# Kernel tuning notes

Measured on AMD Instinct MI355X. Metric: run time of the kernel, lower is better.

The kernel has to match this reference:

```python
import jax, jax.numpy as jnp
import numpy as np

BLOCK = (16, 16)  # (block rows over out_features, block cols over in_features)
TOKENS, IN_F, OUT_F = 8192, 4096, 4096


def setup_inputs() -> dict:
    key = jax.random.key(0)
    k1, k2, k3, k4 = jax.random.split(key, 4)
    x = jax.random.normal(k1, (TOKENS, IN_F), dtype=jnp.float32)
    weight = jax.random.normal(k2, (OUT_F, IN_F), dtype=jnp.float32) / np.sqrt(IN_F)
    bias = jax.random.normal(k3, (OUT_F,), dtype=jnp.float32)
    block_mask = jax.random.bernoulli(k4, 0.5, (OUT_F // BLOCK[0], IN_F // BLOCK[1]))
    return {"x": x, "weight": weight, "bias": bias, "block_mask": block_mask}


def _expand_mask(block_mask, dtype):
    # [X, Y] block mask -> [out_features, in_features] dense 0/1 mask
    m = jnp.repeat(block_mask, BLOCK[0], axis=0)
    m = jnp.repeat(m, BLOCK[1], axis=1)
    return m.astype(dtype)


def reference(x, weight, bias, block_mask):
    # Sparse path: block-sparse matmul with the block-masked weight
    # (blocksparseMM(sparse_data, x, block_size) == x @ (W * mask).T)
    w_sparse = weight * _expand_mask(block_mask, weight.dtype)
    x_sparse = jnp.einsum('ti,oi->to', x, w_sparse)
    # Dense residual path: standard linear with the full weight + bias
    x_dense = jnp.einsum('ti,oi->to', x, weight) + bias
    return x_sparse + x_dense
```

## Files before the change

### kernel.cpp

```cpp
#include <hip/hip_runtime.h>
#include <hip/hip_bf16.h>
#include <stdint.h>

#define TOKENS 8192
#define IN_F   4096
#define OUT_F  4096

typedef __attribute__((ext_vector_type(4))) float  f32x4;
typedef __attribute__((ext_vector_type(8))) __bf16 bf16x8;

__device__ __forceinline__ unsigned short f2bf(float f) {
    union { float f; uint32_t u; } c; c.f = f;
    uint32_t u = c.u;
    u += 0x7fffu + ((u >> 16) & 1);
    return (unsigned short)(u >> 16);
}

__device__ __forceinline__ void load_lds_16(const void* gptr, void* lptr) {
    __builtin_amdgcn_global_load_lds(
        (const __attribute__((address_space(1))) unsigned int*)gptr,
        (__attribute__((address_space(3))) unsigned int*)lptr, 16, 0, 0);
}

template<int N> __device__ __forceinline__ void vm_bar() {
    if constexpr (N == 6)      asm volatile("s_waitcnt vmcnt(6)\ns_barrier" ::: "memory");
    else if constexpr (N == 5) asm volatile("s_waitcnt vmcnt(5)\ns_barrier" ::: "memory");
    else if constexpr (N == 4) asm volatile("s_waitcnt vmcnt(4)\ns_barrier" ::: "memory");
    else if constexpr (N == 3) asm volatile("s_waitcnt vmcnt(3)\ns_barrier" ::: "memory");
    else if constexpr (N == 2) asm volatile("s_waitcnt vmcnt(2)\ns_barrier" ::: "memory");
    else if constexpr (N == 1) asm volatile("s_waitcnt vmcnt(1)\ns_barrier" ::: "memory");
    else                       asm volatile("s_waitcnt vmcnt(0)\ns_barrier" ::: "memory");
}

__global__ __launch_bounds__(256) void cvt_x_kernel(const float* __restrict__ x,
                                                    unsigned short* __restrict__ xb, int n4) {
    int i = blockIdx.x * blockDim.x + threadIdx.x;
    int stride = gridDim.x * blockDim.x;
    for (; i < n4; i += stride) {
        float4 v = ((const float4*)x)[i];
        ushort4 o;
        o.x = f2bf(v.x); o.y = f2bf(v.y); o.z = f2bf(v.z); o.w = f2bf(v.w);
        ((ushort4*)xb)[i] = o;
    }
}

__global__ __launch_bounds__(256) void cvt_w_kernel(const float* __restrict__ w,
                                                    const int* __restrict__ mask,
                                                    unsigned short* __restrict__ wb) {
    const int n4 = OUT_F * IN_F / 4;
    int i = blockIdx.x * blockDim.x + threadIdx.x;
    int stride = gridDim.x * blockDim.x;
    for (; i < n4; i += stride) {
        int elem = i * 4;
        int o = elem >> 12;
        int k = elem & (IN_F - 1);
        int mb = mask[(o >> 4) * (IN_F / 16) + (k >> 4)];
        float s = mb ? 2.0f : 1.0f;
        float4 v = ((const float4*)w)[i];
        ushort4 ov;
        ov.x = f2bf(v.x * s); ov.y = f2bf(v.y * s);
        ov.z = f2bf(v.z * s); ov.w = f2bf(v.w * s);
        ((ushort4*)wb)[i] = ov;
    }
}

#define BM 256
#define BN 256
#define BK 64
#define TILE_SH (BM * BK)

#define PHASE_MFMA(P)                                                          \
    {                                                                          \
        bf16x8 b0 = *(const bf16x8*)(pB + boff0 + (P) * 1024);                 \
        bf16x8 b1 = *(const bf16x8*)(pB + boff1 + (P) * 1024);                 \
        __builtin_amdgcn_s_setprio(1);                                         \
        _Pragma("unroll")                                                      \
        for (int mf = 0; mf < 8; ++mf) {                                       \
            acc[mf][P] = __builtin_amdgcn_mfma_f32_16x16x32_bf16(a[mf][0], b0, acc[mf][P], 0, 0, 0); \
            acc[mf][P] = __builtin_amdgcn_mfma_f32_16x16x32_bf16(a[mf][1], b1, acc[mf][P], 0, 0, 0); \
        }                                                                      \
        __builtin_amdgcn_s_setprio(0);                                         \
    }

#define KTILE(STG, V0, V1, V2, V3)                                             \
    {                                                                          \
        vm_bar<V0>();                                                          \
        if (STG) {                                                             \
            load_lds_16(cgA, stA + dA);                                        \
            load_lds_16(cgA + (size_t)64 * IN_F, stA + dA + 4096);             \
        }                                                                      \
        _Pragma("unroll")                                                      \
        for (int mf = 0; mf < 8; ++mf) {                                       \
            a[mf][0] = *(const bf16x8*)(pA + aoff0 + mf * 1024);               \
            a[mf][1] = *(const bf16x8*)(pA + aoff1 + mf * 1024);               \
        }                                                                      \
        PHASE_MFMA(0)                                                          \
        vm_bar<V1>();                                                          \
        if (STG) {                                                             \
            load_lds_16(cgA + (size_t)128 * IN_F, stA + dA + 8192);            \
            load_lds_16(cgA + (size_t)192 * IN_F, stA + dA + 12288);           \
        }                                                                      \
        PHASE_MFMA(1)                                                          \
        vm_bar<V2>();                                                          \
        if (STG) {                                                             \
            load_lds_16(cgB, stB + dB);                                        \
            load_lds_16(cgB + (size_t)16 * IN_F, stB + dB + 1024);             \
        }                                                                      \
        PHASE_MFMA(2)                                                          \
        vm_bar<V3>();                                                          \
        if (STG) {                                                             \
            load_lds_16(cgB + (size_t)32 * IN_F, stB + dB + 2048);             \
            load_lds_16(cgB + (size_t)48 * IN_F, stB + dB + 3072);             \
        }                                                                      \
        PHASE_MFMA(3)                                                          \
    }

__global__ __launch_bounds__(512, 2) void gemm8_kernel(const unsigned short* __restrict__ A,
                                                       const unsigned short* __restrict__ B,
                                                       const float* __restrict__ bias,
                                                       float* __restrict__ C) {
    extern __shared__ __align__(16) unsigned short sm[];

    const int tid  = threadIdx.x;
    const int lane = tid & 63;
    const int wid  = tid >> 6;
    const int wr   = wid >> 2;
    const int wc   = wid & 3;

    const int nwg = (TOKENS / BM) * (OUT_F / BN);
    int bid = blockIdx.x;
    int swz = (bid & 7) * (nwg >> 3) + (bid >> 3);
    const int tiles_n = OUT_F / BN;
    const int t0 = (swz / tiles_n) * BM;
    const int o0 = (swz % tiles_n) * BN;

    const int srow = tid >> 3;
    const int lc   = (tid & 7) ^ (srow & 7);
    const unsigned short* gA = A + (size_t)(t0 + srow) * IN_F + lc * 8;
    const int growb = (wid >> 1) * 64 + (wid & 1) * 8 + (lane >> 3);
    const unsigned short* gB = B + (size_t)(o0 + growb) * IN_F + lc * 8;
    const int dA = tid * 8;
    const int dB = growb * 64 + (tid & 7) * 8;

    const int l15 = lane & 15, q = lane >> 4, l7 = lane & 7;
    const int aoff0 = (wr * 128 + l15) * 64 + (q ^ l7) * 8;
    const int aoff1 = (wr * 128 + l15) * 64 + ((4 + q) ^ l7) * 8;
    const int boff0 = (wc * 64 + l15) * 64 + (q ^ l7) * 8;
    const int boff1 = (wc * 64 + l15) * 64 + ((4 + q) ^ l7) * 8;

    f32x4 acc[8][4];
#pragma unroll
    for (int i = 0; i < 8; ++i)
#pragma unroll
        for (int j = 0; j < 4; ++j) acc[i][j] = (f32x4)0.0f;

#pragma unroll
    for (int r = 0; r < 4; ++r)
        load_lds_16(gA + (size_t)r * 64 * IN_F, sm + dA + r * 4096);
#pragma unroll
    for (int j = 0; j < 4; ++j)
        load_lds_16(gB + (size_t)j * 16 * IN_F, sm + 2 * TILE_SH + dB + j * 1024);

    bf16x8 a[8][2];

    const unsigned short* cgA = gA + BK;
    const unsigned short* cgB = gB + BK;
    for (int kt = 0; kt < IN_F / BK - 1; ++kt) {
        const int cur = kt & 1, nxt = (kt + 1) & 1;
        const unsigned short* pA = sm + cur * TILE_SH;
        const unsigned short* pB = sm + 2 * TILE_SH + cur * TILE_SH;
        unsigned short* stA = sm + nxt * TILE_SH;
        unsigned short* stB = sm + 2 * TILE_SH + nxt * TILE_SH;
        KTILE(true, 3, 4, 5, 6)
        cgA += BK; cgB += BK;
    }
    {
        const unsigned short* pA = sm + TILE_SH;
        const unsigned short* pB = sm + 2 * TILE_SH + TILE_SH;
        unsigned short* stA = sm;
        unsigned short* stB = sm + 2 * TILE_SH;
        KTILE(false, 3, 2, 1, 0)
        (void)stA; (void)stB;
    }

    float bv[4];
#pragma unroll
    for (int nf = 0; nf < 4; ++nf) bv[nf] = bias[o0 + wc * 64 + nf * 16 + l15];
#pragma unroll
    for (int mf = 0; mf < 8; ++mf) {
        const int t = t0 + wr * 128 + mf * 16 + q * 4;
#pragma unroll
        for (int nf = 0; nf < 4; ++nf) {
            const int o = o0 + wc * 64 + nf * 16 + l15;
#pragma unroll
            for (int r = 0; r < 4; ++r)
                C[(size_t)(t + r) * OUT_F + o] = acc[mf][nf][r] + bv[nf];
        }
    }
}

__global__ __launch_bounds__(256) void gemm_f32_fallback(const float* __restrict__ x,
                                                         const float* __restrict__ w,
                                                         const float* __restrict__ bias,
                                                         const int* __restrict__ mask,
                                                         float* __restrict__ out) {
    __shared__ float As[64][17];
    __shared__ float Bs[64][17];
    int bid = blockIdx.x;
    const int tiles_n = OUT_F / 64;
    int tm = bid / tiles_n, tn = bid % tiles_n;
    int t0 = tm * 64, o0 = tn * 64;
    int tid = threadIdx.x;
    int tx = tid & 15, ty = tid >> 4;
    int lrow = tid >> 2, lc4 = (tid & 3) * 4;
    float acc[4][4] = {};
    for (int k0 = 0; k0 < IN_F; k0 += 16) {
        float4 av = *(const float4*)&x[(size_t)(t0 + lrow) * IN_F + k0 + lc4];
        float4 bv = *(const float4*)&w[(size_t)(o0 + lrow) * IN_F + k0 + lc4];
        int mb = mask[((o0 + lrow) >> 4) * (IN_F / 16) + ((k0 + lc4) >> 4)];
        float s = mb ? 2.0f : 1.0f;
        As[lrow][lc4 + 0] = av.x; As[lrow][lc4 + 1] = av.y;
        As[lrow][lc4 + 2] = av.z; As[lrow][lc4 + 3] = av.w;
        Bs[lrow][lc4 + 0] = bv.x * s; Bs[lrow][lc4 + 1] = bv.y * s;
        Bs[lrow][lc4 + 2] = bv.z * s; Bs[lrow][lc4 + 3] = bv.w * s;
        __syncthreads();
#pragma unroll
        for (int kk = 0; kk < 16; ++kk) {
            float av2[4], bv2[4];
#pragma unroll
            for (int i = 0; i < 4; ++i) av2[i] = As[ty * 4 + i][kk];
#pragma unroll
            for (int j = 0; j < 4; ++j) bv2[j] = Bs[tx * 4 + j][kk];
#pragma unroll
            for (int i = 0; i < 4; ++i)
#pragma unroll
                for (int j = 0; j < 4; ++j) acc[i][j] += av2[i] * bv2[j];
        }
        __syncthreads();
    }
#pragma unroll
    for (int j = 0; j < 4; ++j) {
        int o = o0 + tx * 4 + j;
        float bv = bias[o];
#pragma unroll
        for (int i = 0; i < 4; ++i)
            out[(size_t)(t0 + ty * 4 + i) * OUT_F + o] = acc[i][j] + bv;
    }
}

extern "C" void kernel_launch(void* const* d_in, const int* in_sizes, int n_in,
                              void* d_out, int out_size, void* d_ws, size_t ws_size,
                              hipStream_t stream) {
    const float* x    = (const float*)d_in[0];
    const float* wgt  = (const float*)d_in[1];
    const float* bias = (const float*)d_in[2];
    const int*   mask = (const int*)d_in[3];
    float* out = (float*)d_out;

    size_t xb_bytes = (size_t)TOKENS * IN_F * 2;
    size_t wb_bytes = (size_t)OUT_F * IN_F * 2;

    if (ws_size >= xb_bytes + wb_bytes) {
        unsigned short* xb = (unsigned short*)d_ws;
        unsigned short* wb = (unsigned short*)((char*)d_ws + xb_bytes);
        hipLaunchKernelGGL(cvt_x_kernel, dim3(2048), dim3(256), 0, stream, x, xb, TOKENS * IN_F / 4);
        hipLaunchKernelGGL(cvt_w_kernel, dim3(1024), dim3(256), 0, stream, wgt, mask, wb);
        (void)hipFuncSetAttribute((const void*)gemm8_kernel,
                                  hipFuncAttributeMaxDynamicSharedMemorySize, 131072);
        hipLaunchKernelGGL(gemm8_kernel, dim3((TOKENS / BM) * (OUT_F / BN)), dim3(512),
                           131072, stream, xb, wb, bias, out);
    } else {
        hipLaunchKernelGGL(gemm_f32_fallback, dim3((TOKENS / 64) * (OUT_F / 64)), dim3(256), 0, stream,
                           x, wgt, bias, mask, out);
    }
}
```

Baseline: 280.0 us.

## Restructure GEMM main loop into half-K sub-tiles with finer-grained LDS pipeline

Reorganizes the LDS layout into 32-wide K halves with a new XOR swizzle. The main loop becomes a ping-pong schedule: each sub-step issues fragment reads, then the async global-to-LDS load for a future half-tile, then 16 MFMAs fenced by barriers, keeping three half-tiles in flight. The aim is to hide global latency and LDS reads behind MFMA work while cutting register pressure from the previously held 16 A fragments. It adds many more barriers per K-tile, which could cost synchronization overhead.

```diff
diff --git a/kernel.cpp b/kernel.cpp
--- a/kernel.cpp
+++ b/kernel.cpp
@@ -22,13 +22,14 @@
         (__attribute__((address_space(3))) unsigned int*)lptr, 16, 0, 0);
 }
 
-template<int N> __device__ __forceinline__ void vm_bar() {
-    if constexpr (N == 6)      asm volatile("s_waitcnt vmcnt(6)\ns_barrier" ::: "memory");
-    else if constexpr (N == 5) asm volatile("s_waitcnt vmcnt(5)\ns_barrier" ::: "memory");
-    else if constexpr (N == 4) asm volatile("s_waitcnt vmcnt(4)\ns_barrier" ::: "memory");
-    else if constexpr (N == 3) asm volatile("s_waitcnt vmcnt(3)\ns_barrier" ::: "memory");
-    else if constexpr (N == 2) asm volatile("s_waitcnt vmcnt(2)\ns_barrier" ::: "memory");
-    else if constexpr (N == 1) asm volatile("s_waitcnt vmcnt(1)\ns_barrier" ::: "memory");
+__device__ __forceinline__ void open_bar() {
+    asm volatile("s_barrier\ns_waitcnt lgkmcnt(0)" ::: "memory");
+    __builtin_amdgcn_sched_barrier(0);
+}
+__device__ __forceinline__ void cbar() { asm volatile("s_barrier" ::: "memory"); }
+template<int W> __device__ __forceinline__ void cbar_w() {
+    if constexpr (W == 8)      asm volatile("s_waitcnt vmcnt(8)\ns_barrier" ::: "memory");
+    else if constexpr (W == 4) asm volatile("s_waitcnt vmcnt(4)\ns_barrier" ::: "memory");
     else                       asm volatile("s_waitcnt vmcnt(0)\ns_barrier" ::: "memory");
 }
 
@@ -67,53 +68,64 @@
 #define BM 256
 #define BN 256
 #define BK 64
-#define TILE_SH (BM * BK)
-
-#define PHASE_MFMA(P)                                                          \
-    {                                                                          \
-        bf16x8 b0 = *(const bf16x8*)(pB + boff0 + (P) * 1024);                 \
-        bf16x8 b1 = *(const bf16x8*)(pB + boff1 + (P) * 1024);                 \
-        __builtin_amdgcn_s_setprio(1);                                         \
-        _Pragma("unroll")                                                      \
-        for (int mf = 0; mf < 8; ++mf) {                                       \
-            acc[mf][P] = __builtin_amdgcn_mfma_f32_16x16x32_bf16(a[mf][0], b0, acc[mf][P], 0, 0, 0); \
-            acc[mf][P] = __builtin_amdgcn_mfma_f32_16x16x32_bf16(a[mf][1], b1, acc[mf][P], 0, 0, 0); \
-        }                                                                      \
-        __builtin_amdgcn_s_setprio(0);                                         \
-    }
-
-#define KTILE(STG, V0, V1, V2, V3)                                             \
-    {                                                                          \
-        vm_bar<V0>();                                                          \
-        if (STG) {                                                             \
-            load_lds_16(cgA, stA + dA);                                        \
-            load_lds_16(cgA + (size_t)64 * IN_F, stA + dA + 4096);             \
-        }                                                                      \
-        _Pragma("unroll")                                                      \
-        for (int mf = 0; mf < 8; ++mf) {                                       \
-            a[mf][0] = *(const bf16x8*)(pA + aoff0 + mf * 1024);               \
-            a[mf][1] = *(const bf16x8*)(pA + aoff1 + mf * 1024);               \
-        }                                                                      \
-        PHASE_MFMA(0)                                                          \
-        vm_bar<V1>();                                                          \
-        if (STG) {                                                             \
-            load_lds_16(cgA + (size_t)128 * IN_F, stA + dA + 8192);            \
-            load_lds_16(cgA + (size_t)192 * IN_F, stA + dA + 12288);           \
-        }                                                                      \
-        PHASE_MFMA(1)                                                          \
-        vm_bar<V2>();                                                          \
-        if (STG) {                                                             \
-            load_lds_16(cgB, stB + dB);                                        \
-            load_lds_16(cgB + (size_t)16 * IN_F, stB + dB + 1024);             \
-        }                                                                      \
-        PHASE_MFMA(2)                                                          \
-        vm_bar<V3>();                                                          \
-        if (STG) {                                                             \
-            load_lds_16(cgB + (size_t)32 * IN_F, stB + dB + 2048);             \
-            load_lds_16(cgB + (size_t)48 * IN_F, stB + dB + 3072);             \
-        }                                                                      \
-        PHASE_MFMA(3)                                                          \
-    }
+#define NT (IN_F / BK)
+
+#define RD_B(KS) {                                                             \
+    const unsigned short* pB_ = sm + 32768 + bcur * 16384 + (KS) * 8192 + b_base; \
+    bb0 = *(const bf16x8*)(pB_);        bb1 = *(const bf16x8*)(pB_ + 512);     \
+    bb2 = *(const bf16x8*)(pB_ + 1024); bb3 = *(const bf16x8*)(pB_ + 1536); }
+
+#define RD_A(KS, MH) {                                                         \
+    const unsigned short* pA_ = sm + bcur * 16384 + (KS) * 8192 + a_base + (MH) * 2048; \
+    aa0 = *(const bf16x8*)(pA_);        aa1 = *(const bf16x8*)(pA_ + 512);     \
+    aa2 = *(const bf16x8*)(pA_ + 1024); aa3 = *(const bf16x8*)(pA_ + 1536); }
+
+#define MM16(MH) {                                                             \
+    __builtin_amdgcn_s_setprio(1);                                             \
+    acc[(MH)*4+0][0] = __builtin_amdgcn_mfma_f32_16x16x32_bf16(aa0, bb0, acc[(MH)*4+0][0], 0, 0, 0); \
+    acc[(MH)*4+0][1] = __builtin_amdgcn_mfma_f32_16x16x32_bf16(aa0, bb1, acc[(MH)*4+0][1], 0, 0, 0); \
+    acc[(MH)*4+0][2] = __builtin_amdgcn_mfma_f32_16x16x32_bf16(aa0, bb2, acc[(MH)*4+0][2], 0, 0, 0); \
+    acc[(MH)*4+0][3] = __builtin_amdgcn_mfma_f32_16x16x32_bf16(aa0, bb3, acc[(MH)*4+0][3], 0, 0, 0); \
+    acc[(MH)*4+1][0] = __builtin_amdgcn_mfma_f32_16x16x32_bf16(aa1, bb0, acc[(MH)*4+1][0], 0, 0, 0); \
+    acc[(MH)*4+1][1] = __builtin_amdgcn_mfma_f32_16x16x32_bf16(aa1, bb1, acc[(MH)*4+1][1], 0, 0, 0); \
+    acc[(MH)*4+1][2] = __builtin_amdgcn_mfma_f32_16x16x32_bf16(aa1, bb2, acc[(MH)*4+1][2], 0, 0, 0); \
+    acc[(MH)*4+1][3] = __builtin_amdgcn_mfma_f32_16x16x32_bf16(aa1, bb3, acc[(MH)*4+1][3], 0, 0, 0); \
+    acc[(MH)*4+2][0] = __builtin_amdgcn_mfma_f32_16x16x32_bf16(aa2, bb0, acc[(MH)*4+2][0], 0, 0, 0); \
+    acc[(MH)*4+2][1] = __builtin_amdgcn_mfma_f32_16x16x32_bf16(aa2, bb1, acc[(MH)*4+2][1], 0, 0, 0); \
+    acc[(MH)*4+2][2] = __builtin_amdgcn_mfma_f32_16x16x32_bf16(aa2, bb2, acc[(MH)*4+2][2], 0, 0, 0); \
+    acc[(MH)*4+2][3] = __builtin_amdgcn_mfma_f32_16x16x32_bf16(aa2, bb3, acc[(MH)*4+2][3], 0, 0, 0); \
+    acc[(MH)*4+3][0] = __builtin_amdgcn_mfma_f32_16x16x32_bf16(aa3, bb0, acc[(MH)*4+3][0], 0, 0, 0); \
+    acc[(MH)*4+3][1] = __builtin_amdgcn_mfma_f32_16x16x32_bf16(aa3, bb1, acc[(MH)*4+3][1], 0, 0, 0); \
+    acc[(MH)*4+3][2] = __builtin_amdgcn_mfma_f32_16x16x32_bf16(aa3, bb2, acc[(MH)*4+3][2], 0, 0, 0); \
+    acc[(MH)*4+3][3] = __builtin_amdgcn_mfma_f32_16x16x32_bf16(aa3, bb3, acc[(MH)*4+3][3], 0, 0, 0); \
+    __builtin_amdgcn_s_setprio(0); }
+
+#define ST_A(T, H) {                                                           \
+    const unsigned short* s_ = srcA + (size_t)(T) * 64 + (H) * 32;             \
+    unsigned short* d_ = sm + (((T) & 1) * 16384 + (H) * 8192) + dstA;         \
+    load_lds_16(s_, d_);                                                       \
+    load_lds_16(s_ + (size_t)128 * IN_F, d_ + 4096); }
+#define ST_B(T, H) {                                                           \
+    const unsigned short* s_ = srcB + (size_t)(T) * 64 + (H) * 32;             \
+    unsigned short* d_ = sm + (32768 + ((T) & 1) * 16384 + (H) * 8192) + dstB; \
+    load_lds_16(s_, d_);                                                       \
+    load_lds_16(s_ + (size_t)128 * IN_F, d_ + 4096); }
+
+#define KTILE(S1, S2, W1, W3, TN)                                              \
+  {                                                                            \
+    RD_B(0) RD_A(0, 0)                                                         \
+    if (S1) ST_A(TN, 1)                                                        \
+    open_bar(); MM16(0) cbar();                                                \
+    RD_A(0, 1)                                                                 \
+    if (S1) ST_B(TN, 1)                                                        \
+    open_bar(); MM16(1) cbar_w<W1>();                                          \
+    RD_B(1) RD_A(1, 0)                                                         \
+    if (S2) ST_A((TN) + 1, 0)                                                  \
+    open_bar(); MM16(0) cbar();                                                \
+    RD_A(1, 1)                                                                 \
+    if (S2) ST_B((TN) + 1, 0)                                                  \
+    open_bar(); MM16(1) cbar_w<W3>();                                          \
+  }
 
 __global__ __launch_bounds__(512, 2) void gemm8_kernel(const unsigned short* __restrict__ A,
                                                        const unsigned short* __restrict__ B,
@@ -134,19 +146,18 @@
     const int t0 = (swz / tiles_n) * BM;
     const int o0 = (swz % tiles_n) * BN;
 
-    const int srow = tid >> 3;
-    const int lc   = (tid & 7) ^ (srow & 7);
-    const unsigned short* gA = A + (size_t)(t0 + srow) * IN_F + lc * 8;
-    const int growb = (wid >> 1) * 64 + (wid & 1) * 8 + (lane >> 3);
-    const unsigned short* gB = B + (size_t)(o0 + growb) * IN_F + lc * 8;
-    const int dA = tid * 8;
-    const int dB = growb * 64 + (tid & 7) * 8;
-
-    const int l15 = lane & 15, q = lane >> 4, l7 = lane & 7;
-    const int aoff0 = (wr * 128 + l15) * 64 + (q ^ l7) * 8;
-    const int aoff1 = (wr * 128 + l15) * 64 + ((4 + q) ^ l7) * 8;
-    const int boff0 = (wc * 64 + l15) * 64 + (q ^ l7) * 8;
-    const int boff1 = (wc * 64 + l15) * 64 + ((4 + q) ^ l7) * 8;
+    const int srow = tid >> 2;
+    const int sc   = tid & 3;
+    const int scs  = sc ^ ((srow >> 1) & 3);
+    const unsigned short* srcA = A + (size_t)(t0 + srow) * IN_F + scs * 8;
+    const unsigned short* srcB = B + (size_t)(o0 + srow) * IN_F + scs * 8;
+    const int dstA = srow * 32 + sc * 8;
+    const int dstB = dstA;
+
+    const int l15 = lane & 15, q = lane >> 4;
+    const int qe = q ^ ((l15 >> 1) & 3);
+    const int a_base = (wr * 128 + l15) * 32 + qe * 8;
+    const int b_base = (wc * 64 + l15) * 32 + qe * 8;
 
     f32x4 acc[8][4];
 #pragma unroll
@@ -154,33 +165,22 @@
 #pragma unroll
         for (int j = 0; j < 4; ++j) acc[i][j] = (f32x4)0.0f;
 
-#pragma unroll
-    for (int r = 0; r < 4; ++r)
-        load_lds_16(gA + (size_t)r * 64 * IN_F, sm + dA + r * 4096);
-#pragma unroll
-    for (int j = 0; j < 4; ++j)
-        load_lds_16(gB + (size_t)j * 16 * IN_F, sm + 2 * TILE_SH + dB + j * 1024);
-
-    bf16x8 a[8][2];
-
-    const unsigned short* cgA = gA + BK;
-    const unsigned short* cgB = gB + BK;
-    for (int kt = 0; kt < IN_F / BK - 1; ++kt) {
-        const int cur = kt & 1, nxt = (kt + 1) & 1;
-        const unsigned short* pA = sm + cur * TILE_SH;
-        const unsigned short* pB = sm + 2 * TILE_SH + cur * TILE_SH;
-        unsigned short* stA = sm + nxt * TILE_SH;
-        unsigned short* stB = sm + 2 * TILE_SH + nxt * TILE_SH;
-        KTILE(true, 3, 4, 5, 6)
-        cgA += BK; cgB += BK;
-    }
-    {
-        const unsigned short* pA = sm + TILE_SH;
-        const unsigned short* pB = sm + 2 * TILE_SH + TILE_SH;
-        unsigned short* stA = sm;
-        unsigned short* stB = sm + 2 * TILE_SH;
-        KTILE(false, 3, 2, 1, 0)
-        (void)stA; (void)stB;
+    bf16x8 aa0, aa1, aa2, aa3, bb0, bb1, bb2, bb3;
+
+    ST_A(0, 0) ST_B(0, 0)
+    ST_A(0, 1) ST_B(0, 1)
+    ST_A(1, 0) ST_B(1, 0)
+    cbar_w<8>();
+
+    for (int kt = 0; kt < NT - 2; ++kt) {
+        const int bcur = kt & 1;
+        KTILE(true, true, 8, 8, kt + 1)
+    }
+    {   const int bcur = (NT - 2) & 1;
+        KTILE(true, false, 8, 4, NT - 1)
+    }
+    {   const int bcur = (NT - 1) & 1;
+        KTILE(false, false, 0, 0, NT)
     }
 
     float bv[4];
```

Result: slower. 294.4 us (+5.1%).
